# Optimization experiments

Measured on AMD Instinct MI355X. Metric: run time of the kernel, lower is better.

## Reference

```python
import jax, jax.numpy as jnp
import numpy as np

N = 100000
IN_CH, HID_CH, OUT_CH = 128, 128, 64
E = 1600000


def gcn_layer(x, W, b, src, dst, num_nodes):
    """PyG GCNConv: add self-loops, symmetric deg^-1/2 normalization,
    x' = D^-1/2 (A+I) D^-1/2 (x W) + b."""
    # degrees including self-loops (deg = 1 + in-degree with unit edge weights)
    ones = jnp.ones(dst.shape[0], dtype=x.dtype)
    deg = jnp.ones(num_nodes, dtype=x.dtype).at[dst].add(ones)
    dinv = jax.lax.rsqrt(deg)
    h = x @ W  # [N, out_dim] -- transform before propagate (PyG order)
    # neighbor messages
    norm = dinv[src] * dinv[dst]                      # [E]
    msg = h[src] * norm[:, None]                      # [E, out_dim] (traffic-bound)
    agg = jax.ops.segment_sum(msg, dst, num_segments=num_nodes)
    # self-loop contribution: norm_ii = dinv[i]^2
    agg = agg + h * (dinv * dinv)[:, None]
    return agg + b


def setup_inputs() -> dict:
    key = jax.random.key(0)
    ks = jax.random.split(key, 7)
    x = jax.random.normal(ks[0], (N, IN_CH), dtype=jnp.float32)
    edge_index = jax.random.randint(ks[1], (2, E), 0, N, dtype=jnp.int64)
    # Glorot-style init like PyG GCNConv
    W1 = jax.random.normal(ks[2], (IN_CH, HID_CH), dtype=jnp.float32) * (1.0 / np.sqrt(IN_CH))
    b1 = jnp.zeros((HID_CH,), dtype=jnp.float32)
    W2 = jax.random.normal(ks[3], (HID_CH, OUT_CH), dtype=jnp.float32) * (1.0 / np.sqrt(HID_CH))
    b2 = jnp.zeros((OUT_CH,), dtype=jnp.float32)
    return {"x": x, "edge_index": edge_index, "W1": W1, "b1": b1, "W2": W2, "b2": b2}


def reference(x, edge_index, W1, b1, W2, b2):
    src, dst = edge_index[0], edge_index[1]
    h = gcn_layer(x, W1, b1, src, dst, N)
    h = jax.nn.relu(h)  # dropout is identity in eval mode
    out = gcn_layer(h, W2, b2, src, dst, N)
    return out
```

## Files before the change

kernel.cpp:

```cpp
#include <hip/hip_runtime.h>
#include <hip/hip_fp16.h>

#define NNODES 100000
#define NEDGES 1600000
#define IN_C   128
#define HID_C  128
#define OUT_C  64

#define CAP     64
#define OVF_MAX 4096

#define BUCKET_SHIFT 7
#define BUCKET_NODES 128
#define NB ((NNODES + BUCKET_NODES - 1) / BUCKET_NODES)
#define BCAP 3072
#define BCNT_STRIDE 16
#define EB 4096
#define NBLK_A ((NEDGES + EB - 1) / EB)
#define GB ((NNODES + 63) / 64)

typedef __attribute__((ext_vector_type(8))) _Float16 half8;
typedef __attribute__((ext_vector_type(4))) _Float16 half4;
typedef __attribute__((ext_vector_type(4))) float floatx4;

__device__ __forceinline__ long long load_idx(const void* p, long long i, int is64) {
  return is64 ? ((const long long*)p)[i] : (long long)((const int*)p)[i];
}

__global__ void zero_detect_kernel(const void* eidx, int* flag, int* bcnt,
                                   int* ovf_cnt, int* ovfA_cnt) {
  int i = blockIdx.x * 256 + threadIdx.x;
  if (i < NB * BCNT_STRIDE) bcnt[i] = 0;
  if (i == 0) { *ovf_cnt = 0; *ovfA_cnt = 0; }
  if (blockIdx.x == 0 && threadIdx.x < 64) {
    const unsigned* w = (const unsigned*)eidx;
    unsigned v = w[2 * threadIdx.x + 1];
    unsigned long long bad = __ballot(v != 0u);
    if (threadIdx.x == 0) *flag = (bad == 0ull) ? 1 : 0;
  }
}

__global__ __launch_bounds__(256) void binA_gemm1_kernel(
    const void* __restrict__ eidx, const int* __restrict__ flag,
    int* __restrict__ bcnt, unsigned* __restrict__ buf,
    int* __restrict__ ovfA_cnt, int2* __restrict__ ovfA,
    const float* __restrict__ x, const float* __restrict__ W1,
    _Float16* __restrict__ h1) {
  __shared__ alignas(16) char smem[52224];
  const int tid = threadIdx.x;

  if (blockIdx.x < NBLK_A) {
    unsigned* se = (unsigned*)smem;
    unsigned short* be = (unsigned short*)(smem + 16384);
    int* hist = (int*)(smem + 24576);
    int* base = (int*)(smem + 27712);
    int* ofs  = (int*)(smem + 30848);

    const int e0 = blockIdx.x * EB;
    const int e1 = min(e0 + EB, NEDGES);
    const int m = e1 - e0;
    const int is64 = *flag;

    for (int b = tid; b < NB; b += 256) { hist[b] = 0; ofs[b] = 0; }
    __syncthreads();

    for (int k = tid; k < m; k += 256) {
      int e = e0 + k;
      int s = (int)load_idx(eidx, e, is64);
      int d = (int)load_idx(eidx, (long long)NEDGES + e, is64);
      int b = d >> BUCKET_SHIFT;
      se[k] = (unsigned)s | ((unsigned)(d & (BUCKET_NODES - 1)) << 17);
      be[k] = (unsigned short)b;
      atomicAdd(&hist[b], 1);
    }
    __syncthreads();

    int rot = (blockIdx.x * 131) % NB;
    for (int idx = tid; idx < NB; idx += 256) {
      int b = idx + rot;
      if (b >= NB) b -= NB;
      int h = hist[b];
      if (h > 0) base[b] = atomicAdd(&bcnt[b * BCNT_STRIDE], h);
    }
    __syncthreads();

    for (int k = tid; k < m; k += 256) {
      unsigned u = se[k];
      int b = be[k];
      int ko = atomicAdd(&ofs[b], 1);
      int slot = base[b] + ko;
      if (slot < BCAP) {
        buf[(size_t)b * BCAP + slot] = u;
      } else {
        int p = atomicAdd(ovfA_cnt, 1);
        if (p < OVF_MAX)
          ovfA[p] = make_int2((int)(u & 0x1FFFFu),
                              (b << BUCKET_SHIFT) | (int)(u >> 17));
      }
    }
  } else {
    constexpr int K = IN_C, N = HID_C, KP = K + 8;
    _Float16* Alds = (_Float16*)smem;
    _Float16* Wlds = (_Float16*)(smem + 17408);
    const int row0 = (blockIdx.x - NBLK_A) * 64;

    constexpr int TILES = (K / 4) * (N / 4);
    for (int tile = tid; tile < TILES; tile += 256) {
      int kt = tile / (N / 4);
      int nt = tile % (N / 4);
      const float* wp = &W1[(4 * kt) * N + 4 * nt];
      float4 r0 = *(const float4*)(wp);
      float4 r1 = *(const float4*)(wp + N);
      float4 r2 = *(const float4*)(wp + 2 * N);
      float4 r3 = *(const float4*)(wp + 3 * N);
      half4 c0 = {(_Float16)r0.x, (_Float16)r1.x, (_Float16)r2.x, (_Float16)r3.x};
      half4 c1 = {(_Float16)r0.y, (_Float16)r1.y, (_Float16)r2.y, (_Float16)r3.y};
      half4 c2 = {(_Float16)r0.z, (_Float16)r1.z, (_Float16)r2.z, (_Float16)r3.z};
      half4 c3 = {(_Float16)r0.w, (_Float16)r1.w, (_Float16)r2.w, (_Float16)r3.w};
      *(half4*)&Wlds[(4 * nt + 0) * KP + 4 * kt] = c0;
      *(half4*)&Wlds[(4 * nt + 1) * KP + 4 * kt] = c1;
      *(half4*)&Wlds[(4 * nt + 2) * KP + 4 * kt] = c2;
      *(half4*)&Wlds[(4 * nt + 3) * KP + 4 * kt] = c3;
    }
    constexpr int F4PR = K / 4;
    for (int idx = tid; idx < 64 * F4PR; idx += 256) {
      int lr = idx / F4PR;
      int c4 = (idx % F4PR) * 4;
      int gr = row0 + lr;
      if (gr > NNODES - 1) gr = NNODES - 1;
      float4 v = *(const float4*)&x[(size_t)gr * K + c4];
      half4 h = {(_Float16)v.x, (_Float16)v.y, (_Float16)v.z, (_Float16)v.w};
      *(half4*)&Alds[lr * KP + c4] = h;
    }
    __syncthreads();

    const int w = tid >> 6;
    const int lane = tid & 63;
    const int g = lane >> 4;
    const int mi = lane & 15;
    constexpr int NT = N / 16;
    floatx4 acc[NT];
#pragma unroll
    for (int t = 0; t < NT; ++t) acc[t] = (floatx4){0.f, 0.f, 0.f, 0.f};
    const _Float16* arow = &Alds[(w * 16 + mi) * KP];
#pragma unroll
    for (int ks = 0; ks < K / 32; ++ks) {
      half8 a = *(const half8*)(arow + ks * 32 + g * 8);
#pragma unroll
      for (int t = 0; t < NT; ++t) {
        half8 b = *(const half8*)&Wlds[(t * 16 + mi) * KP + ks * 32 + g * 8];
        acc[t] = __builtin_amdgcn_mfma_f32_16x16x32_f16(a, b, acc[t], 0, 0, 0);
      }
    }
#pragma unroll
    for (int r = 0; r < 4; ++r) {
      int grow = row0 + w * 16 + 4 * g + r;
      if (grow < NNODES) {
        _Float16* orow = h1 + (size_t)grow * N + mi;
#pragma unroll
        for (int t = 0; t < NT; ++t) orow[t * 16] = (_Float16)acc[t][r];
      }
    }
  }
}

__global__ __launch_bounds__(256) void binB_kernel(const int* __restrict__ bcnt,
                                                   const unsigned* __restrict__ buf,
                                                   const int* __restrict__ ovfA_cnt,
                                                   const int2* __restrict__ ovfA,
                                                   int* __restrict__ cnt,
                                                   float* __restrict__ dinv,
                                                   int* __restrict__ pad_csr,
                                                   int* __restrict__ ovf_cnt,
                                                   int2* __restrict__ ovf) {
  __shared__ int pad[BUCKET_NODES * CAP];
  __shared__ int lcnt[BUCKET_NODES];
  const int b = blockIdx.x;
  const int tid = threadIdx.x;
  const int node0 = b << BUCKET_SHIFT;

  if (tid < BUCKET_NODES) lcnt[tid] = 0;
  __syncthreads();

  const int n = min(bcnt[b * BCNT_STRIDE], BCAP);
  for (int k = tid; k < n; k += 256) {
    unsigned u = buf[(size_t)b * BCAP + k];
    int s = (int)(u & 0x1FFFFu);
    int dl = (int)(u >> 17);
    int slot = atomicAdd(&lcnt[dl], 1);
    if (slot < CAP) {
      pad[dl * CAP + slot] = s;
    } else {
      int p = atomicAdd(ovf_cnt, 1);
      if (p < OVF_MAX) ovf[p] = make_int2(s, node0 + dl);
    }
  }
  int na = min(*ovfA_cnt, OVF_MAX);
  for (int t = tid; t < na; t += 256) {
    int2 p = ovfA[t];
    if ((p.y >> BUCKET_SHIFT) == b) {
      int dl = p.y & (BUCKET_NODES - 1);
      int slot = atomicAdd(&lcnt[dl], 1);
      if (slot < CAP) {
        pad[dl * CAP + slot] = p.x;
      } else {
        int q = atomicAdd(ovf_cnt, 1);
        if (q < OVF_MAX) ovf[q] = make_int2(p.x, p.y);
      }
    }
  }
  __syncthreads();

  constexpr int I4PN = CAP / 4;
  for (int q = tid; q < BUCKET_NODES * I4PN; q += 256) {
    int dl = q / I4PN;
    int gn = node0 + dl;
    if (gn < NNODES) {
      int c = (q % I4PN) * 4;
      *(int4*)&pad_csr[(size_t)gn * CAP + c] = *(const int4*)&pad[dl * CAP + c];
    }
  }
  if (tid < BUCKET_NODES && node0 + tid < NNODES) {
    int c = lcnt[tid];
    cnt[node0 + tid] = c;
    dinv[node0 + tid] = rsqrtf((float)(c + 1));
  }
}

struct F8 {
  float x0, x1, x2, x3, x4, x5, x6, x7;
};

__device__ __forceinline__ void add_h8s(F8& a, const __half* p, float s) {
  int4 r = *(const int4*)p;
  const __half2* h = (const __half2*)&r;
  float2 f0 = __half22float2(h[0]);
  float2 f1 = __half22float2(h[1]);
  float2 f2 = __half22float2(h[2]);
  float2 f3 = __half22float2(h[3]);
  a.x0 = fmaf(s, f0.x, a.x0); a.x1 = fmaf(s, f0.y, a.x1);
  a.x2 = fmaf(s, f1.x, a.x2); a.x3 = fmaf(s, f1.y, a.x3);
  a.x4 = fmaf(s, f2.x, a.x4); a.x5 = fmaf(s, f2.y, a.x5);
  a.x6 = fmaf(s, f3.x, a.x6); a.x7 = fmaf(s, f3.y, a.x7);
}

__global__ __launch_bounds__(512) void gather1_gemm2_kernel(
    const int* __restrict__ cnt, const int* __restrict__ pad_csr,
    const float* __restrict__ dinv, const __half* __restrict__ h1,
    const float* __restrict__ b1, const float* __restrict__ W2,
    const int* __restrict__ ovf_cnt, const int2* __restrict__ ovf,
    _Float16* __restrict__ h2) {
  constexpr int K = HID_C, N = OUT_C, KP = K + 8;
  __shared__ alignas(16) _Float16 Hl[64 * KP];
  __shared__ alignas(16) _Float16 W2l[N * KP];
  const int tid = threadIdx.x;
  const int node0 = blockIdx.x * 64;

  constexpr int TILES = (K / 4) * (N / 4);
  for (int tile = tid; tile < TILES; tile += 512) {
    int kt = tile / (N / 4);
    int nt = tile % (N / 4);
    const float* wp = &W2[(4 * kt) * N + 4 * nt];
    float4 r0 = *(const float4*)(wp);
    float4 r1 = *(const float4*)(wp + N);
    float4 r2 = *(const float4*)(wp + 2 * N);
    float4 r3 = *(const float4*)(wp + 3 * N);
    half4 c0 = {(_Float16)r0.x, (_Float16)r1.x, (_Float16)r2.x, (_Float16)r3.x};
    half4 c1 = {(_Float16)r0.y, (_Float16)r1.y, (_Float16)r2.y, (_Float16)r3.y};
    half4 c2 = {(_Float16)r0.z, (_Float16)r1.z, (_Float16)r2.z, (_Float16)r3.z};
    half4 c3 = {(_Float16)r0.w, (_Float16)r1.w, (_Float16)r2.w, (_Float16)r3.w};
    *(half4*)&W2l[(4 * nt + 0) * KP + 4 * kt] = c0;
    *(half4*)&W2l[(4 * nt + 1) * KP + 4 * kt] = c1;
    *(half4*)&W2l[(4 * nt + 2) * KP + 4 * kt] = c2;
    *(half4*)&W2l[(4 * nt + 3) * KP + 4 * kt] = c3;
  }

  const int il = tid >> 3;
  const int c16 = (tid & 7) * 16;
  const int i = node0 + il;

  float o[16];
#pragma unroll
  for (int q = 0; q < 16; ++q) o[q] = 0.f;

  if (i < NNODES) {
    const float di = dinv[i];
    const int deg = cnt[i];
    const int beg = i * CAP;
    const int end = beg + min(deg, CAP);
    const int* __restrict__ lst = pad_csr;
    const __half* __restrict__ Hb = h1 + c16;

    F8 a0l = {}, a0h = {}, a1l = {}, a1h = {};
    {
      const __half* p = Hb + (size_t)i * K;
      add_h8s(a0l, p, di);
      add_h8s(a0h, p + 8, di);
    }
    int j = beg;
    for (; j + 8 <= end; j += 8) {
      int4 sa = *(const int4*)&lst[j];
      int4 sb = *(const int4*)&lst[j + 4];
      float d0 = dinv[sa.x], d1 = dinv[sa.y], d2 = dinv[sa.z], d3 = dinv[sa.w];
      float d4 = dinv[sb.x], d5 = dinv[sb.y], d6 = dinv[sb.z], d7 = dinv[sb.w];
      const __half* p0 = Hb + (size_t)sa.x * K;
      const __half* p1 = Hb + (size_t)sa.y * K;
      const __half* p2 = Hb + (size_t)sa.z * K;
      const __half* p3 = Hb + (size_t)sa.w * K;
      add_h8s(a0l, p0, d0); add_h8s(a0h, p0 + 8, d0);
      add_h8s(a1l, p1, d1); add_h8s(a1h, p1 + 8, d1);
      add_h8s(a0l, p2, d2); add_h8s(a0h, p2 + 8, d2);
      add_h8s(a1l, p3, d3); add_h8s(a1h, p3 + 8, d3);
      const __half* p4 = Hb + (size_t)sb.x * K;
      const __half* p5 = Hb + (size_t)sb.y * K;
      const __half* p6 = Hb + (size_t)sb.z * K;
      const __half* p7 = Hb + (size_t)sb.w * K;
      add_h8s(a0l, p4, d4); add_h8s(a0h, p4 + 8, d4);
      add_h8s(a1l, p5, d5); add_h8s(a1h, p5 + 8, d5);
      add_h8s(a0l, p6, d6); add_h8s(a0h, p6 + 8, d6);
      add_h8s(a1l, p7, d7); add_h8s(a1h, p7 + 8, d7);
    }
    for (; j < end; ++j) {
      int s = lst[j];
      float ds = dinv[s];
      const __half* p0 = Hb + (size_t)s * K;
      add_h8s(a0l, p0, ds); add_h8s(a0h, p0 + 8, ds);
    }
    if (deg > CAP) {
      int nv = min(*ovf_cnt, OVF_MAX);
      for (int t = 0; t < nv; ++t) {
        int2 p = ovf[t];
        if (p.y == i) {
          float ds = dinv[p.x];
          const __half* q = Hb + (size_t)p.x * K;
          add_h8s(a0l, q, ds); add_h8s(a0h, q + 8, ds);
        }
      }
    }
    float4 bb0 = *(const float4*)&b1[c16];
    float4 bb1 = *(const float4*)&b1[c16 + 4];
    float4 bb2 = *(const float4*)&b1[c16 + 8];
    float4 bb3 = *(const float4*)&b1[c16 + 12];
    o[0] = fmaf(a0l.x0 + a1l.x0, di, bb0.x);
    o[1] = fmaf(a0l.x1 + a1l.x1, di, bb0.y);
    o[2] = fmaf(a0l.x2 + a1l.x2, di, bb0.z);
    o[3] = fmaf(a0l.x3 + a1l.x3, di, bb0.w);
    o[4] = fmaf(a0l.x4 + a1l.x4, di, bb1.x);
    o[5] = fmaf(a0l.x5 + a1l.x5, di, bb1.y);
    o[6] = fmaf(a0l.x6 + a1l.x6, di, bb1.z);
    o[7] = fmaf(a0l.x7 + a1l.x7, di, bb1.w);
    o[8] = fmaf(a0h.x0 + a1h.x0, di, bb2.x);
    o[9] = fmaf(a0h.x1 + a1h.x1, di, bb2.y);
    o[10] = fmaf(a0h.x2 + a1h.x2, di, bb2.z);
    o[11] = fmaf(a0h.x3 + a1h.x3, di, bb2.w);
    o[12] = fmaf(a0h.x4 + a1h.x4, di, bb3.x);
    o[13] = fmaf(a0h.x5 + a1h.x5, di, bb3.y);
    o[14] = fmaf(a0h.x6 + a1h.x6, di, bb3.z);
    o[15] = fmaf(a0h.x7 + a1h.x7, di, bb3.w);
#pragma unroll
    for (int q = 0; q < 16; ++q) o[q] = o[q] > 0.f ? o[q] : 0.f;
  }
  {
    half8 hv0 = {(_Float16)o[0], (_Float16)o[1], (_Float16)o[2], (_Float16)o[3],
                 (_Float16)o[4], (_Float16)o[5], (_Float16)o[6], (_Float16)o[7]};
    half8 hv1 = {(_Float16)o[8], (_Float16)o[9], (_Float16)o[10], (_Float16)o[11],
                 (_Float16)o[12], (_Float16)o[13], (_Float16)o[14], (_Float16)o[15]};
    *(half8*)&Hl[il * KP + c16] = hv0;
    *(half8*)&Hl[il * KP + c16 + 8] = hv1;
  }
  __syncthreads();

  const int w = tid >> 6;
  const int lane = tid & 63;
  const int g = lane >> 4;
  const int mi = lane & 15;
  const int wrow = (w & 3) * 16;
  const int wcol = (w >> 2) * 32;

  floatx4 acc[2];
  acc[0] = (floatx4){0.f, 0.f, 0.f, 0.f};
  acc[1] = (floatx4){0.f, 0.f, 0.f, 0.f};
  const _Float16* arow = &Hl[(wrow + mi) * KP];
#pragma unroll
  for (int ks = 0; ks < K / 32; ++ks) {
    half8 a = *(const half8*)(arow + ks * 32 + g * 8);
#pragma unroll
    for (int t = 0; t < 2; ++t) {
      half8 b = *(const half8*)&W2l[(wcol + t * 16 + mi) * KP + ks * 32 + g * 8];
      acc[t] = __builtin_amdgcn_mfma_f32_16x16x32_f16(a, b, acc[t], 0, 0, 0);
    }
  }
#pragma unroll
  for (int r = 0; r < 4; ++r) {
    int grow = node0 + wrow + 4 * g + r;
    if (grow < NNODES) {
      _Float16* orow = h2 + (size_t)grow * N + wcol + mi;
#pragma unroll
      for (int t = 0; t < 2; ++t) orow[t * 16] = (_Float16)acc[t][r];
    }
  }
}

__global__ __launch_bounds__(256) void gather2_kernel(
    const int* __restrict__ cnt, const int* __restrict__ pad_csr,
    const float* __restrict__ dinv, const __half* __restrict__ h2,
    const float* __restrict__ b2, const int* __restrict__ ovf_cnt,
    const int2* __restrict__ ovf, float* __restrict__ Out) {
  constexpr int C = OUT_C;
  constexpr int TPN = C / 16;
  int gid = blockIdx.x * 256 + threadIdx.x;
  int i = gid / TPN;
  int c16 = (gid % TPN) * 16;
  if (i >= NNODES) return;

  const float di = dinv[i];
  const int deg = cnt[i];
  const int beg = i * CAP;
  const int end = beg + min(deg, CAP);
  const int* __restrict__ lst = pad_csr;
  const __half* __restrict__ Hb = h2 + c16;

  F8 a0l = {}, a0h = {}, a1l = {}, a1h = {};
  {
    const __half* p = Hb + (size_t)i * C;
    add_h8s(a0l, p, di);
    add_h8s(a0h, p + 8, di);
  }
  int j = beg;
  for (; j + 8 <= end; j += 8) {
    int4 sa = *(const int4*)&lst[j];
    int4 sb = *(const int4*)&lst[j + 4];
    float d0 = dinv[sa.x], d1 = dinv[sa.y], d2 = dinv[sa.z], d3 = dinv[sa.w];
    float d4 = dinv[sb.x], d5 = dinv[sb.y], d6 = dinv[sb.z], d7 = dinv[sb.w];
    const __half* p0 = Hb + (size_t)sa.x * C;
    const __half* p1 = Hb + (size_t)sa.y * C;
    const __half* p2 = Hb + (size_t)sa.z * C;
    const __half* p3 = Hb + (size_t)sa.w * C;
    add_h8s(a0l, p0, d0); add_h8s(a0h, p0 + 8, d0);
    add_h8s(a1l, p1, d1); add_h8s(a1h, p1 + 8, d1);
    add_h8s(a0l, p2, d2); add_h8s(a0h, p2 + 8, d2);
    add_h8s(a1l, p3, d3); add_h8s(a1h, p3 + 8, d3);
    const __half* p4 = Hb + (size_t)sb.x * C;
    const __half* p5 = Hb + (size_t)sb.y * C;
    const __half* p6 = Hb + (size_t)sb.z * C;
    const __half* p7 = Hb + (size_t)sb.w * C;
    add_h8s(a0l, p4, d4); add_h8s(a0h, p4 + 8, d4);
    add_h8s(a1l, p5, d5); add_h8s(a1h, p5 + 8, d5);
    add_h8s(a0l, p6, d6); add_h8s(a0h, p6 + 8, d6);
    add_h8s(a1l, p7, d7); add_h8s(a1h, p7 + 8, d7);
  }
  for (; j < end; ++j) {
    int s = lst[j];
    float ds = dinv[s];
    const __half* p0 = Hb + (size_t)s * C;
    add_h8s(a0l, p0, ds); add_h8s(a0h, p0 + 8, ds);
  }
  if (deg > CAP) {
    int nv = min(*ovf_cnt, OVF_MAX);
    for (int t = 0; t < nv; ++t) {
      int2 p = ovf[t];
      if (p.y == i) {
        float ds = dinv[p.x];
        const __half* q = Hb + (size_t)p.x * C;
        add_h8s(a0l, q, ds); add_h8s(a0h, q + 8, ds);
      }
    }
  }

  float4 bb0 = *(const float4*)&b2[c16];
  float4 bb1 = *(const float4*)&b2[c16 + 4];
  float4 bb2 = *(const float4*)&b2[c16 + 8];
  float4 bb3 = *(const float4*)&b2[c16 + 12];
  float* O = Out + (size_t)i * C + c16;
  *(float4*)O = make_float4(fmaf(a0l.x0 + a1l.x0, di, bb0.x),
                            fmaf(a0l.x1 + a1l.x1, di, bb0.y),
                            fmaf(a0l.x2 + a1l.x2, di, bb0.z),
                            fmaf(a0l.x3 + a1l.x3, di, bb0.w));
  *(float4*)(O + 4) = make_float4(fmaf(a0l.x4 + a1l.x4, di, bb1.x),
                                  fmaf(a0l.x5 + a1l.x5, di, bb1.y),
                                  fmaf(a0l.x6 + a1l.x6, di, bb1.z),
                                  fmaf(a0l.x7 + a1l.x7, di, bb1.w));
  *(float4*)(O + 8) = make_float4(fmaf(a0h.x0 + a1h.x0, di, bb2.x),
                                  fmaf(a0h.x1 + a1h.x1, di, bb2.y),
                                  fmaf(a0h.x2 + a1h.x2, di, bb2.z),
                                  fmaf(a0h.x3 + a1h.x3, di, bb2.w));
  *(float4*)(O + 12) = make_float4(fmaf(a0h.x4 + a1h.x4, di, bb3.x),
                                   fmaf(a0h.x5 + a1h.x5, di, bb3.y),
                                   fmaf(a0h.x6 + a1h.x6, di, bb3.z),
                                   fmaf(a0h.x7 + a1h.x7, di, bb3.w));
}

extern "C" void kernel_launch(void* const* d_in, const int* in_sizes, int n_in,
                              void* d_out, int out_size, void* d_ws, size_t ws_size,
                              hipStream_t stream) {
  const float* x = (const float*)d_in[0];
  const void* eidx = d_in[1];
  const float* W1 = (const float*)d_in[2];
  const float* b1 = (const float*)d_in[3];
  const float* W2 = (const float*)d_in[4];
  const float* b2 = (const float*)d_in[5];
  float* out = (float*)d_out;
  char* ws = (char*)d_ws;

  int*      flag     = (int*)(ws + 0);
  int*      ovf_cnt  = (int*)(ws + 512);
  int*      ovfA_cnt = (int*)(ws + 1024);
  int*      bcnt     = (int*)(ws + 1536);
  int*      cnt      = (int*)(ws + 52224);
  float*    dinv     = (float*)(ws + 452608);
  int2*     ovf      = (int2*)(ws + 852992);
  int2*     ovfA     = (int2*)(ws + 885760);
  unsigned* buf      = (unsigned*)(ws + 918528);
  int*      pad_csr  = (int*)(ws + 10528256);
  _Float16* h1       = (_Float16*)(ws + 36128256);
  _Float16* h2       = (_Float16*)(ws + 61728256);

  zero_detect_kernel<<<(NB * BCNT_STRIDE + 255) / 256, 256, 0, stream>>>(
      eidx, flag, bcnt, ovf_cnt, ovfA_cnt);
  binA_gemm1_kernel<<<NBLK_A + GB, 256, 0, stream>>>(eidx, flag, bcnt, buf,
                                                     ovfA_cnt, ovfA, x, W1, h1);
  binB_kernel<<<NB, 256, 0, stream>>>(bcnt, buf, ovfA_cnt, ovfA, cnt, dinv,
                                      pad_csr, ovf_cnt, ovf);
  gather1_gemm2_kernel<<<GB, 512, 0, stream>>>(cnt, pad_csr, dinv,
                                               (const __half*)h1, b1, W2,
                                               ovf_cnt, ovf, h2);
  gather2_kernel<<<(NNODES * (OUT_C / 16) + 255) / 256, 256, 0, stream>>>(
      cnt, pad_csr, dinv, (const __half*)h2, b2, ovf_cnt, ovf, out);
}
```

Measured before the change: 277.2 us.

## Pre-scale GEMM outputs by dinv so gathers skip per-neighbor dinv loads

Splits the fused binning+GEMM1 kernel so GEMM1 runs after dinv is known, then folds the source-side dinv scaling into the GEMM1 and GEMM2 epilogues. The gather kernels then do plain fp16 sums with no random dinv[src] loads or per-neighbor multiplies, and the tail loop is unrolled by two. The cost is an extra launch and losing the overlap between binning and GEMM1. Scaling before the fp16 store also changes rounding slightly.

```diff
diff --git a/kernel.cpp b/kernel.cpp
--- a/kernel.cpp
+++ b/kernel.cpp
@@ -40,126 +40,58 @@
   }
 }
 
-__global__ __launch_bounds__(256) void binA_gemm1_kernel(
-    const void* __restrict__ eidx, const int* __restrict__ flag,
-    int* __restrict__ bcnt, unsigned* __restrict__ buf,
-    int* __restrict__ ovfA_cnt, int2* __restrict__ ovfA,
-    const float* __restrict__ x, const float* __restrict__ W1,
-    _Float16* __restrict__ h1) {
-  __shared__ alignas(16) char smem[52224];
+__global__ __launch_bounds__(256) void binA_kernel(const void* __restrict__ eidx,
+                                                   const int* __restrict__ flag,
+                                                   int* __restrict__ bcnt,
+                                                   unsigned* __restrict__ buf,
+                                                   int* __restrict__ ovfA_cnt,
+                                                   int2* __restrict__ ovfA) {
+  __shared__ unsigned se[EB];
+  __shared__ unsigned short be[EB];
+  __shared__ int hist[NB];
+  __shared__ int base[NB];
+  __shared__ int ofs[NB];
   const int tid = threadIdx.x;
-
-  if (blockIdx.x < NBLK_A) {
-    unsigned* se = (unsigned*)smem;
-    unsigned short* be = (unsigned short*)(smem + 16384);
-    int* hist = (int*)(smem + 24576);
-    int* base = (int*)(smem + 27712);
-    int* ofs  = (int*)(smem + 30848);
-
-    const int e0 = blockIdx.x * EB;
-    const int e1 = min(e0 + EB, NEDGES);
-    const int m = e1 - e0;
-    const int is64 = *flag;
-
-    for (int b = tid; b < NB; b += 256) { hist[b] = 0; ofs[b] = 0; }
-    __syncthreads();
-
-    for (int k = tid; k < m; k += 256) {
-      int e = e0 + k;
-      int s = (int)load_idx(eidx, e, is64);
-      int d = (int)load_idx(eidx, (long long)NEDGES + e, is64);
-      int b = d >> BUCKET_SHIFT;
-      se[k] = (unsigned)s | ((unsigned)(d & (BUCKET_NODES - 1)) << 17);
-      be[k] = (unsigned short)b;
-      atomicAdd(&hist[b], 1);
-    }
-    __syncthreads();
-
-    int rot = (blockIdx.x * 131) % NB;
-    for (int idx = tid; idx < NB; idx += 256) {
-      int b = idx + rot;
-      if (b >= NB) b -= NB;
-      int h = hist[b];
-      if (h > 0) base[b] = atomicAdd(&bcnt[b * BCNT_STRIDE], h);
-    }
-    __syncthreads();
-
-    for (int k = tid; k < m; k += 256) {
-      unsigned u = se[k];
-      int b = be[k];
-      int ko = atomicAdd(&ofs[b], 1);
-      int slot = base[b] + ko;
-      if (slot < BCAP) {
-        buf[(size_t)b * BCAP + slot] = u;
-      } else {
-        int p = atomicAdd(ovfA_cnt, 1);
-        if (p < OVF_MAX)
-          ovfA[p] = make_int2((int)(u & 0x1FFFFu),
-                              (b << BUCKET_SHIFT) | (int)(u >> 17));
-      }
-    }
-  } else {
-    constexpr int K = IN_C, N = HID_C, KP = K + 8;
-    _Float16* Alds = (_Float16*)smem;
-    _Float16* Wlds = (_Float16*)(smem + 17408);
-    const int row0 = (blockIdx.x - NBLK_A) * 64;
-
-    constexpr int TILES = (K / 4) * (N / 4);
-    for (int tile = tid; tile < TILES; tile += 256) {
-      int kt = tile / (N / 4);
-      int nt = tile % (N / 4);
-      const float* wp = &W1[(4 * kt) * N + 4 * nt];
-      float4 r0 = *(const float4*)(wp);
-      float4 r1 = *(const float4*)(wp + N);
-      float4 r2 = *(const float4*)(wp + 2 * N);
-      float4 r3 = *(const float4*)(wp + 3 * N);
-      half4 c0 = {(_Float16)r0.x, (_Float16)r1.x, (_Float16)r2.x, (_Float16)r3.x};
-      half4 c1 = {(_Float16)r0.y, (_Float16)r1.y, (_Float16)r2.y, (_Float16)r3.y};
-      half4 c2 = {(_Float16)r0.z, (_Float16)r1.z, (_Float16)r2.z, (_Float16)r3.z};
-      half4 c3 = {(_Float16)r0.w, (_Float16)r1.w, (_Float16)r2.w, (_Float16)r3.w};
-      *(half4*)&Wlds[(4 * nt + 0) * KP + 4 * kt] = c0;
-      *(half4*)&Wlds[(4 * nt + 1) * KP + 4 * kt] = c1;
-      *(half4*)&Wlds[(4 * nt + 2) * KP + 4 * kt] = c2;
-      *(half4*)&Wlds[(4 * nt + 3) * KP + 4 * kt] = c3;
-    }
-    constexpr int F4PR = K / 4;
-    for (int idx = tid; idx < 64 * F4PR; idx += 256) {
-      int lr = idx / F4PR;
-      int c4 = (idx % F4PR) * 4;
-      int gr = row0 + lr;
-      if (gr > NNODES - 1) gr = NNODES - 1;
-      float4 v = *(const float4*)&x[(size_t)gr * K + c4];
-      half4 h = {(_Float16)v.x, (_Float16)v.y, (_Float16)v.z, (_Float16)v.w};
-      *(half4*)&Alds[lr * KP + c4] = h;
-    }
-    __syncthreads();
-
-    const int w = tid >> 6;
-    const int lane = tid & 63;
-    const int g = lane >> 4;
-    const int mi = lane & 15;
-    constexpr int NT = N / 16;
-    floatx4 acc[NT];
-#pragma unroll
-    for (int t = 0; t < NT; ++t) acc[t] = (floatx4){0.f, 0.f, 0.f, 0.f};
-    const _Float16* arow = &Alds[(w * 16 + mi) * KP];
-#pragma unroll
-    for (int ks = 0; ks < K / 32; ++ks) {
-      half8 a = *(const half8*)(arow + ks * 32 + g * 8);
-#pragma unroll
-      for (int t = 0; t < NT; ++t) {
-        half8 b = *(const half8*)&Wlds[(t * 16 + mi) * KP + ks * 32 + g * 8];
-        acc[t] = __builtin_amdgcn_mfma_f32_16x16x32_f16(a, b, acc[t], 0, 0, 0);
-      }
-    }
-#pragma unroll
-    for (int r = 0; r < 4; ++r) {
-      int grow = row0 + w * 16 + 4 * g + r;
-      if (grow < NNODES) {
-        _Float16* orow = h1 + (size_t)grow * N + mi;
-#pragma unroll
-        for (int t = 0; t < NT; ++t) orow[t * 16] = (_Float16)acc[t][r];
-      }
+  const int e0 = blockIdx.x * EB;
+  const int e1 = min(e0 + EB, NEDGES);
+  const int m = e1 - e0;
+  const int is64 = *flag;
+
+  for (int b = tid; b < NB; b += 256) { hist[b] = 0; ofs[b] = 0; }
+  __syncthreads();
+
+  for (int k = tid; k < m; k += 256) {
+    int e = e0 + k;
+    int s = (int)load_idx(eidx, e, is64);
+    int d = (int)load_idx(eidx, (long long)NEDGES + e, is64);
+    int b = d >> BUCKET_SHIFT;
+    se[k] = (unsigned)s | ((unsigned)(d & (BUCKET_NODES - 1)) << 17);
+    be[k] = (unsigned short)b;
+    atomicAdd(&hist[b], 1);
+  }
+  __syncthreads();
+
+  int rot = (blockIdx.x * 131) % NB;
+  for (int idx = tid; idx < NB; idx += 256) {
+    int b = idx + rot;
+    if (b >= NB) b -= NB;
+    int h = hist[b];
+    if (h > 0) base[b] = atomicAdd(&bcnt[b * BCNT_STRIDE], h);
+  }
+  __syncthreads();
+
+  for (int k = tid; k < m; k += 256) {
+    unsigned u = se[k];
+    int b = be[k];
+    int ko = atomicAdd(&ofs[b], 1);
+    int slot = base[b] + ko;
+    if (slot < BCAP) {
+      buf[(size_t)b * BCAP + slot] = u;
+    } else {
+      int p = atomicAdd(ovfA_cnt, 1);
+      if (p < OVF_MAX)
+        ovfA[p] = make_int2((int)(u & 0x1FFFFu),
+                            (b << BUCKET_SHIFT) | (int)(u >> 17));
     }
   }
 }
@@ -227,29 +159,97 @@
   }
 }
 
+__global__ __launch_bounds__(256) void gemm1_kernel(const float* __restrict__ x,
+                                                    const float* __restrict__ W1,
+                                                    const float* __restrict__ dinv,
+                                                    _Float16* __restrict__ h1s) {
+  constexpr int K = IN_C, N = HID_C, KP = K + 8;
+  __shared__ alignas(16) _Float16 Alds[64 * KP];
+  __shared__ alignas(16) _Float16 Wlds[N * KP];
+  const int tid = threadIdx.x;
+  const int row0 = blockIdx.x * 64;
+
+  constexpr int TILES = (K / 4) * (N / 4);
+  for (int tile = tid; tile < TILES; tile += 256) {
+    int kt = tile & (K / 4 - 1);
+    int nt = tile >> 5;
+    const float* wp = &W1[(4 * kt) * N + 4 * nt];
+    float4 r0 = *(const float4*)(wp);
+    float4 r1 = *(const float4*)(wp + N);
+    float4 r2 = *(const float4*)(wp + 2 * N);
+    float4 r3 = *(const float4*)(wp + 3 * N);
+    half4 c0 = {(_Float16)r0.x, (_Float16)r1.x, (_Float16)r2.x, (_Float16)r3.x};
+    half4 c1 = {(_Float16)r0.y, (_Float16)r1.y, (_Float16)r2.y, (_Float16)r3.y};
+    half4 c2 = {(_Float16)r0.z, (_Float16)r1.z, (_Float16)r2.z, (_Float16)r3.z};
+    half4 c3 = {(_Float16)r0.w, (_Float16)r1.w, (_Float16)r2.w, (_Float16)r3.w};
+    *(half4*)&Wlds[(4 * nt + 0) * KP + 4 * kt] = c0;
+    *(half4*)&Wlds[(4 * nt + 1) * KP + 4 * kt] = c1;
+    *(half4*)&Wlds[(4 * nt + 2) * KP + 4 * kt] = c2;
+    *(half4*)&Wlds[(4 * nt + 3) * KP + 4 * kt] = c3;
+  }
+  constexpr int F4PR = K / 4;
+  for (int idx = tid; idx < 64 * F4PR; idx += 256) {
+    int lr = idx >> 5;
+    int c4 = (idx & 31) * 4;
+    int gr = row0 + lr;
+    if (gr > NNODES - 1) gr = NNODES - 1;
+    float4 v = *(const float4*)&x[(size_t)gr * K + c4];
+    half4 h = {(_Float16)v.x, (_Float16)v.y, (_Float16)v.z, (_Float16)v.w};
+    *(half4*)&Alds[lr * KP + c4] = h;
+  }
+  __syncthreads();
+
+  const int w = tid >> 6;
+  const int lane = tid & 63;
+  const int g = lane >> 4;
+  const int mi = lane & 15;
+  constexpr int NT = N / 16;
+  floatx4 acc[NT];
+#pragma unroll
+  for (int t = 0; t < NT; ++t) acc[t] = (floatx4){0.f, 0.f, 0.f, 0.f};
+  const _Float16* arow = &Alds[(w * 16 + mi) * KP];
+#pragma unroll
+  for (int ks = 0; ks < K / 32; ++ks) {
+    half8 a = *(const half8*)(arow + ks * 32 + g * 8);
+#pragma unroll
+    for (int t = 0; t < NT; ++t) {
+      half8 b = *(const half8*)&Wlds[(t * 16 + mi) * KP + ks * 32 + g * 8];
+      acc[t] = __builtin_amdgcn_mfma_f32_16x16x32_f16(a, b, acc[t], 0, 0, 0);
+    }
+  }
+#pragma unroll
+  for (int r = 0; r < 4; ++r) {
+    int grow = row0 + w * 16 + 4 * g + r;
+    if (grow < NNODES) {
+      float s = dinv[grow];
+      _Float16* orow = h1s + (size_t)grow * N + mi;
+#pragma unroll
+      for (int t = 0; t < NT; ++t) orow[t * 16] = (_Float16)(acc[t][r] * s);
+    }
+  }
+}
+
 struct F8 {
   float x0, x1, x2, x3, x4, x5, x6, x7;
 };
 
-__device__ __forceinline__ void add_h8s(F8& a, const __half* p, float s) {
+__device__ __forceinline__ void add_h8(F8& a, const __half* p) {
   int4 r = *(const int4*)p;
   const __half2* h = (const __half2*)&r;
   float2 f0 = __half22float2(h[0]);
   float2 f1 = __half22float2(h[1]);
   float2 f2 = __half22float2(h[2]);
   float2 f3 = __half22float2(h[3]);
-  a.x0 = fmaf(s, f0.x, a.x0); a.x1 = fmaf(s, f0.y, a.x1);
-  a.x2 = fmaf(s, f1.x, a.x2); a.x3 = fmaf(s, f1.y, a.x3);
-  a.x4 = fmaf(s, f2.x, a.x4); a.x5 = fmaf(s, f2.y, a.x5);
-  a.x6 = fmaf(s, f3.x, a.x6); a.x7 = fmaf(s, f3.y, a.x7);
+  a.x0 += f0.x; a.x1 += f0.y; a.x2 += f1.x; a.x3 += f1.y;
+  a.x4 += f2.x; a.x5 += f2.y; a.x6 += f3.x; a.x7 += f3.y;
 }
 
 __global__ __launch_bounds__(512) void gather1_gemm2_kernel(
     const int* __restrict__ cnt, const int* __restrict__ pad_csr,
-    const float* __restrict__ dinv, const __half* __restrict__ h1,
+    const float* __restrict__ dinv, const __half* __restrict__ Hs1,
     const float* __restrict__ b1, const float* __restrict__ W2,
     const int* __restrict__ ovf_cnt, const int2* __restrict__ ovf,
-    _Float16* __restrict__ h2) {
+    _Float16* __restrict__ h2s) {
   constexpr int K = HID_C, N = OUT_C, KP = K + 8;
   __shared__ alignas(16) _Float16 Hl[64 * KP];
   __shared__ alignas(16) _Float16 W2l[N * KP];
@@ -258,8 +258,8 @@
 
   constexpr int TILES = (K / 4) * (N / 4);
   for (int tile = tid; tile < TILES; tile += 512) {
-    int kt = tile / (N / 4);
-    int nt = tile % (N / 4);
+    int kt = tile & (K / 4 - 1);
+    int nt = tile >> 5;
     const float* wp = &W2[(4 * kt) * N + 4 * nt];
     float4 r0 = *(const float4*)(wp);
     float4 r1 = *(const float4*)(wp + N);
@@ -289,51 +289,52 @@
     const int beg = i * CAP;
     const int end = beg + min(deg, CAP);
     const int* __restrict__ lst = pad_csr;
-    const __half* __restrict__ Hb = h1 + c16;
+    const __half* __restrict__ Hb = Hs1 + c16;
 
     F8 a0l = {}, a0h = {}, a1l = {}, a1h = {};
     {
       const __half* p = Hb + (size_t)i * K;
-      add_h8s(a0l, p, di);
-      add_h8s(a0h, p + 8, di);
+      add_h8(a0l, p);
+      add_h8(a0h, p + 8);
     }
     int j = beg;
     for (; j + 8 <= end; j += 8) {
       int4 sa = *(const int4*)&lst[j];
       int4 sb = *(const int4*)&lst[j + 4];
-      float d0 = dinv[sa.x], d1 = dinv[sa.y], d2 = dinv[sa.z], d3 = dinv[sa.w];
-      float d4 = dinv[sb.x], d5 = dinv[sb.y], d6 = dinv[sb.z], d7 = dinv[sb.w];
       const __half* p0 = Hb + (size_t)sa.x * K;
       const __half* p1 = Hb + (size_t)sa.y * K;
       const __half* p2 = Hb + (size_t)sa.z * K;
       const __half* p3 = Hb + (size_t)sa.w * K;
-      add_h8s(a0l, p0, d0); add_h8s(a0h, p0 + 8, d0);
-      add_h8s(a1l, p1, d1); add_h8s(a1h, p1 + 8, d1);
-      add_h8s(a0l, p2, d2); add_h8s(a0h, p2 + 8, d2);
-      add_h8s(a1l, p3, d3); add_h8s(a1h, p3 + 8, d3);
+      add_h8(a0l, p0); add_h8(a0h, p0 + 8);
+      add_h8(a1l, p1); add_h8(a1h, p1 + 8);
+      add_h8(a0l, p2); add_h8(a0h, p2 + 8);
+      add_h8(a1l, p3); add_h8(a1h, p3 + 8);
       const __half* p4 = Hb + (size_t)sb.x * K;
       const __half* p5 = Hb + (size_t)sb.y * K;
       const __half* p6 = Hb + (size_t)sb.z * K;
       const __half* p7 = Hb + (size_t)sb.w * K;
-      add_h8s(a0l, p4, d4); add_h8s(a0h, p4 + 8, d4);
-      add_h8s(a1l, p5, d5); add_h8s(a1h, p5 + 8, d5);
-      add_h8s(a0l, p6, d6); add_h8s(a0h, p6 + 8, d6);
-      add_h8s(a1l, p7, d7); add_h8s(a1h, p7 + 8, d7);
-    }
-    for (; j < end; ++j) {
-      int s = lst[j];
-      float ds = dinv[s];
-      const __half* p0 = Hb + (size_t)s * K;
-      add_h8s(a0l, p0, ds); add_h8s(a0h, p0 + 8, ds);
+      add_h8(a0l, p4); add_h8(a0h, p4 + 8);
+      add_h8(a1l, p5); add_h8(a1h, p5 + 8);
+      add_h8(a0l, p6); add_h8(a0h, p6 + 8);
+      add_h8(a1l, p7); add_h8(a1h, p7 + 8);
+    }
+    for (; j + 2 <= end; j += 2) {
+      const __half* p0 = Hb + (size_t)lst[j] * K;
+      const __half* p1 = Hb + (size_t)lst[j + 1] * K;
+      add_h8(a0l, p0); add_h8(a0h, p0 + 8);
+      add_h8(a1l, p1); add_h8(a1h, p1 + 8);
+    }
+    if (j < end) {
+      const __half* p0 = Hb + (size_t)lst[j] * K;
+      add_h8(a0l, p0); add_h8(a0h, p0 + 8);
     }
     if (deg > CAP) {
       int nv = min(*ovf_cnt, OVF_MAX);
       for (int t = 0; t < nv; ++t) {
         int2 p = ovf[t];
         if (p.y == i) {
-          float ds = dinv[p.x];
           const __half* q = Hb + (size_t)p.x * K;
-          add_h8s(a0l, q, ds); add_h8s(a0h, q + 8, ds);
+          add_h8(a0l, q); add_h8(a0h, q + 8);
         }
       }
     }
@@ -394,16 +395,17 @@
   for (int r = 0; r < 4; ++r) {
     int grow = node0 + wrow + 4 * g + r;
     if (grow < NNODES) {
-      _Float16* orow = h2 + (size_t)grow * N + wcol + mi;
-#pragma unroll
-      for (int t = 0; t < 2; ++t) orow[t * 16] = (_Float16)acc[t][r];
+      float s = dinv[grow];
+      _Float16* orow = h2s + (size_t)grow * N + wcol + mi;
+#pragma unroll
+      for (int t = 0; t < 2; ++t) orow[t * 16] = (_Float16)(acc[t][r] * s);
     }
   }
 }
 
 __global__ __launch_bounds__(256) void gather2_kernel(
     const int* __restrict__ cnt, const int* __restrict__ pad_csr,
-    const float* __restrict__ dinv, const __half* __restrict__ h2,
+    const float* __restrict__ dinv, const __half* __restrict__ Hs2,
     const float* __restrict__ b2, const int* __restrict__ ovf_cnt,
     const int2* __restrict__ ovf, float* __restrict__ Out) {
   constexpr int C = OUT_C;
@@ -418,51 +420,52 @@
   const int beg = i * CAP;
   const int end = beg + min(deg, CAP);
   const int* __restrict__ lst = pad_csr;
-  const __half* __restrict__ Hb = h2 + c16;
+  const __half* __restrict__ Hb = Hs2 + c16;
 
   F8 a0l = {}, a0h = {}, a1l = {}, a1h = {};
   {
     const __half* p = Hb + (size_t)i * C;
-    add_h8s(a0l, p, di);
-    add_h8s(a0h, p + 8, di);
+    add_h8(a0l, p);
+    add_h8(a0h, p + 8);
   }
   int j = beg;
   for (; j + 8 <= end; j += 8) {
     int4 sa = *(const int4*)&lst[j];
     int4 sb = *(const int4*)&lst[j + 4];
-    float d0 = dinv[sa.x], d1 = dinv[sa.y], d2 = dinv[sa.z], d3 = dinv[sa.w];
-    float d4 = dinv[sb.x], d5 = dinv[sb.y], d6 = dinv[sb.z], d7 = dinv[sb.w];
     const __half* p0 = Hb + (size_t)sa.x * C;
     const __half* p1 = Hb + (size_t)sa.y * C;
     const __half* p2 = Hb + (size_t)sa.z * C;
     const __half* p3 = Hb + (size_t)sa.w * C;
-    add_h8s(a0l, p0, d0); add_h8s(a0h, p0 + 8, d0);
-    add_h8s(a1l, p1, d1); add_h8s(a1h, p1 + 8, d1);
-    add_h8s(a0l, p2, d2); add_h8s(a0h, p2 + 8, d2);
-    add_h8s(a1l, p3, d3); add_h8s(a1h, p3 + 8, d3);
+    add_h8(a0l, p0); add_h8(a0h, p0 + 8);
+    add_h8(a1l, p1); add_h8(a1h, p1 + 8);
+    add_h8(a0l, p2); add_h8(a0h, p2 + 8);
+    add_h8(a1l, p3); add_h8(a1h, p3 + 8);
     const __half* p4 = Hb + (size_t)sb.x * C;
     const __half* p5 = Hb + (size_t)sb.y * C;
     const __half* p6 = Hb + (size_t)sb.z * C;
     const __half* p7 = Hb + (size_t)sb.w * C;
-    add_h8s(a0l, p4, d4); add_h8s(a0h, p4 + 8, d4);
-    add_h8s(a1l, p5, d5); add_h8s(a1h, p5 + 8, d5);
-    add_h8s(a0l, p6, d6); add_h8s(a0h, p6 + 8, d6);
-    add_h8s(a1l, p7, d7); add_h8s(a1h, p7 + 8, d7);
-  }
-  for (; j < end; ++j) {
-    int s = lst[j];
-    float ds = dinv[s];
-    const __half* p0 = Hb + (size_t)s * C;
-    add_h8s(a0l, p0, ds); add_h8s(a0h, p0 + 8, ds);
+    add_h8(a0l, p4); add_h8(a0h, p4 + 8);
+    add_h8(a1l, p5); add_h8(a1h, p5 + 8);
+    add_h8(a0l, p6); add_h8(a0h, p6 + 8);
+    add_h8(a1l, p7); add_h8(a1h, p7 + 8);
+  }
+  for (; j + 2 <= end; j += 2) {
+    const __half* p0 = Hb + (size_t)lst[j] * C;
+    const __half* p1 = Hb + (size_t)lst[j + 1] * C;
+    add_h8(a0l, p0); add_h8(a0h, p0 + 8);
+    add_h8(a1l, p1); add_h8(a1h, p1 + 8);
+  }
+  if (j < end) {
+    const __half* p0 = Hb + (size_t)lst[j] * C;
+    add_h8(a0l, p0); add_h8(a0h, p0 + 8);
   }
   if (deg > CAP) {
     int nv = min(*ovf_cnt, OVF_MAX);
     for (int t = 0; t < nv; ++t) {
       int2 p = ovf[t];
       if (p.y == i) {
-        float ds = dinv[p.x];
         const __half* q = Hb + (size_t)p.x * C;
-        add_h8s(a0l, q, ds); add_h8s(a0h, q + 8, ds);
+        add_h8(a0l, q); add_h8(a0h, q + 8);
       }
     }
   }
@@ -512,18 +515,18 @@
   int2*     ovfA     = (int2*)(ws + 885760);
   unsigned* buf      = (unsigned*)(ws + 918528);
   int*      pad_csr  = (int*)(ws + 10528256);
-  _Float16* h1       = (_Float16*)(ws + 36128256);
-  _Float16* h2       = (_Float16*)(ws + 61728256);
+  _Float16* h1s      = (_Float16*)(ws + 36128256);
+  _Float16* h2s      = (_Float16*)(ws + 61728256);
 
   zero_detect_kernel<<<(NB * BCNT_STRIDE + 255) / 256, 256, 0, stream>>>(
       eidx, flag, bcnt, ovf_cnt, ovfA_cnt);
-  binA_gemm1_kernel<<<NBLK_A + GB, 256, 0, stream>>>(eidx, flag, bcnt, buf,
-                                                     ovfA_cnt, ovfA, x, W1, h1);
+  binA_kernel<<<NBLK_A, 256, 0, stream>>>(eidx, flag, bcnt, buf, ovfA_cnt, ovfA);
   binB_kernel<<<NB, 256, 0, stream>>>(bcnt, buf, ovfA_cnt, ovfA, cnt, dinv,
                                       pad_csr, ovf_cnt, ovf);
+  gemm1_kernel<<<GB, 256, 0, stream>>>(x, W1, dinv, h1s);
   gather1_gemm2_kernel<<<GB, 512, 0, stream>>>(cnt, pad_csr, dinv,
-                                               (const __half*)h1, b1, W2,
-                                               ovf_cnt, ovf, h2);
+                                               (const __half*)h1s, b1, W2,
+                                               ovf_cnt, ovf, h2s);
   gather2_kernel<<<(NNODES * (OUT_C / 16) + 255) / 256, 256, 0, stream>>>(
-      cnt, pad_csr, dinv, (const __half*)h2, b2, ovf_cnt, ovf, out);
-}
+      cnt, pad_csr, dinv, (const __half*)h2s, b2, ovf_cnt, ovf, out);
+}
```

Measured after the change: 281.6 us. Within noise of the previous version (+1.6%).
